# Kernel tuning notes

Measured on AMD Instinct MI355X. Metric: run time of the kernel, lower is better.

Reference implementation:

```python
import jax, jax.numpy as jnp
import numpy as np
import math

IMAGE_C = 1
IMAGE_W = 28
PIXELS_PER_ROW = IMAGE_W * IMAGE_C
NUM_HEADS = 8
TOP_K = 96
WINDOW_SIZE = 128
NEG_INF = -jnp.inf


def _causal_2d_mask(T):
    idx = jnp.arange(T)
    q_i = (idx // PIXELS_PER_ROW)[:, None]
    q_j = (idx % PIXELS_PER_ROW // IMAGE_C)[:, None]
    q_c = (idx % IMAGE_C)[:, None]
    k_i = (idx // PIXELS_PER_ROW)[None, :]
    k_j = (idx % PIXELS_PER_ROW // IMAGE_C)[None, :]
    k_c = (idx % IMAGE_C)[None, :]
    allowed = (k_i < q_i) | ((k_i == q_i) & (k_j < q_j)) | ((k_i == q_i) & (k_j == q_j) & (k_c <= q_c))
    return jnp.where(allowed, 0.0, NEG_INF)[None, None]  # [1,1,T,T]


def _window_mask(T, window_size):
    idx = jnp.arange(T)
    blocked = idx[None, :] < idx[:, None] - window_size + 1
    return jnp.where(blocked, NEG_INF, 0.0)[None, None]  # [1,1,T,T]


def setup_inputs() -> dict:
    key = jax.random.key(0)
    ks = jax.random.split(key, 10)
    B, T, E = 4, 2048, 512
    H = NUM_HEADS
    s = 0.02
    return {
        "x": jax.random.normal(ks[0], (B, T, E), jnp.float32),
        "Wq": jax.random.normal(ks[1], (E, E), jnp.float32) * s,
        "bq": jnp.zeros((E,), jnp.float32),
        "Wk": jax.random.normal(ks[2], (E, E), jnp.float32) * s,
        "bk": jnp.zeros((E,), jnp.float32),
        "Wv": jax.random.normal(ks[3], (E, E), jnp.float32) * s,
        "bv": jnp.zeros((E,), jnp.float32),
        "Wo": jax.random.normal(ks[4], (E, E), jnp.float32) * s,
        "bo": jnp.zeros((E,), jnp.float32),
        "log_sigma": jnp.full((H, 1, 1), math.log(2.5), jnp.float32),
    }


def reference(x, Wq, bq, Wk, bk, Wv, bv, Wo, bo, log_sigma):
    B, T, E = x.shape
    H = NUM_HEADS
    D = E // H

    def split_heads(y):  # [B,T,E] -> [B,H,T,D]
        return y.reshape(B, T, H, D).transpose(0, 2, 1, 3)

    q = split_heads(x @ Wq.T + bq)
    k = split_heads(x @ Wk.T + bk)
    v = split_heads(x @ Wv.T + bv)

    # Gaussian-kernel (squared-distance) scores: ||q-k||^2 / (-2 sigma^2)
    q_sq = jnp.sum(q * q, axis=-1, keepdims=True)            # [B,H,T,1]
    k_sq = jnp.sum(k * k, axis=-1, keepdims=True).transpose(0, 1, 3, 2)  # [B,H,1,T]
    product = jnp.einsum("bhqd,bhkd->bhqk", q, k)
    dist_sq = q_sq + k_sq - 2.0 * product
    sigma_sq = jnp.exp(2.0 * log_sigma)                       # [H,1,1]
    scores = dist_sq / (-2.0 * sigma_sq)

    scores = scores + _causal_2d_mask(T)
    if WINDOW_SIZE < T:
        scores = scores + _window_mask(T, WINDOW_SIZE)

    if TOP_K < T:
        K_val = min(TOP_K, T)
        # keep only the top-K scores per row (threshold at the K-th value);
        # equivalent to torch's gather/scatter for distinct finite scores
        top_vals = jax.lax.top_k(scores, K_val)[0]            # [B,H,T,K]
        kth = top_vals[..., -1:]
        scores = jnp.where(scores >= kth, scores, NEG_INF)

    probs = jax.nn.softmax(scores, axis=-1)                   # dropout = identity (eval)
    out = jnp.einsum("bhqk,bhkd->bhqd", probs, v)
    out = out.transpose(0, 2, 1, 3).reshape(B, T, E)
    return out @ Wo.T + bo
```

## Files before the change

### kernel.cpp

```cpp
#include <hip/hip_runtime.h>
#include <math.h>

#define T_SEQ   2048
#define EDIM    512
#define NHEADS  8
#define DHEAD   64
#define BATCH   4
#define WIN     128
#define TOPK    96

typedef _Float16 f16;
typedef f16 f16x2 __attribute__((ext_vector_type(2)));
typedef f16 f16x4 __attribute__((ext_vector_type(4)));
typedef f16 f16x8 __attribute__((ext_vector_type(8)));
typedef float f32x4 __attribute__((ext_vector_type(4)));

#define GLD_LDS(gp, lp) \
    __builtin_amdgcn_global_load_lds((const __attribute__((address_space(1))) void*)(gp), \
                                     (__attribute__((address_space(3))) void*)(lp), 16, 0, 0)

__global__ __launch_bounds__(256) void convert_all(
    const float* __restrict__ x,  const float* __restrict__ wq,
    const float* __restrict__ wk, const float* __restrict__ wv,
    const float* __restrict__ wo,
    f16* __restrict__ xh, f16* __restrict__ wqkvh, f16* __restrict__ woh)
{
    long i = ((long)blockIdx.x * 256 + threadIdx.x) * 4;
    const float* src; f16* dst; long off;
    if      (i < 4194304L) { src = x;  dst = xh;             off = i;            }
    else if (i < 4456448L) { src = wq; dst = wqkvh;          off = i - 4194304L; }
    else if (i < 4718592L) { src = wk; dst = wqkvh + 262144; off = i - 4456448L; }
    else if (i < 4980736L) { src = wv; dst = wqkvh + 524288; off = i - 4718592L; }
    else                   { src = wo; dst = woh;            off = i - 4980736L; }
    float4 v = *(const float4*)(src + off);
    f16x4 h; h.x = (f16)v.x; h.y = (f16)v.y; h.z = (f16)v.z; h.w = (f16)v.w;
    *(f16x4*)(dst + off) = h;
}

__global__ __launch_bounds__(256) void gemm_qkv(
    const f16* __restrict__ A, const f16* __restrict__ W,
    const float* __restrict__ b0, const float* __restrict__ b1,
    const float* __restrict__ b2,
    f16* __restrict__ cq, f16* __restrict__ ck, f16* __restrict__ cv)
{
    __shared__ f16 SH[16384];
    f16* Ash = SH;
    f16* Bsh = SH + 8192;

    const int tid  = threadIdx.x;
    const int w    = tid >> 6;
    const int lane = tid & 63;
    const int m0   = blockIdx.x * 128;
    const int n0   = blockIdx.y * 128;
    const int K    = 512;
    const int lr   = lane & 15;
    const int lk8  = (lane >> 4) * 8;

    f32x4 acc[4][4];
#pragma unroll
    for (int i = 0; i < 4; i++)
#pragma unroll
        for (int j = 0; j < 4; j++) acc[i][j] = (f32x4){0.f, 0.f, 0.f, 0.f};

    const int wmi = (w & 1) * 4;
    const int wni = (w >> 1) * 4;

    for (int k0 = 0; k0 < K; k0 += 64) {
#pragma unroll
        for (int cc = 0; cc < 4; cc++) {
            const int c  = w * 4 + cc;
            const int ms = c & 7, kp = c >> 3;
            const int kcol = k0 + kp * 32 + lk8;
            GLD_LDS(A + (size_t)(m0 + ms * 16 + lr) * K + kcol, Ash + c * 512);
            GLD_LDS(W + (size_t)(n0 + ms * 16 + lr) * K + kcol, Bsh + c * 512);
        }
        __syncthreads();

#pragma unroll
        for (int kp = 0; kp < 2; kp++) {
            f16x8 af[4], bf[4];
#pragma unroll
            for (int i = 0; i < 4; i++)
                af[i] = *(const f16x8*)(Ash + (kp * 8 + wmi + i) * 512 + lane * 8);
#pragma unroll
            for (int j = 0; j < 4; j++)
                bf[j] = *(const f16x8*)(Bsh + (kp * 8 + wni + j) * 512 + lane * 8);
#pragma unroll
            for (int i = 0; i < 4; i++)
#pragma unroll
                for (int j = 0; j < 4; j++)
                    acc[i][j] = __builtin_amdgcn_mfma_f32_16x16x32_f16(af[i], bf[j], acc[i][j], 0, 0, 0);
        }
        __syncthreads();
    }

    const int quad = lane >> 4;
    const int mat  = n0 >> 9;
    const float* bias = (mat == 0) ? b0 : ((mat == 1) ? b1 : b2);
    const int bb  = m0 >> 11;
    const int t0  = m0 & (T_SEQ - 1);
    const int hh0 = (n0 & 511) >> 6;

    if (mat < 2) {
#pragma unroll
        for (int i = 0; i < 4; i++) {
#pragma unroll
            for (int j = 0; j < 4; j++) {
                const int nl = (w >> 1) * 64 + j * 16 + lr;
                const float bvv = bias[(n0 & 511) + nl];
#pragma unroll
                for (int r = 0; r < 4; r++) {
                    const int ml = (w & 1) * 64 + i * 16 + quad * 4 + r;
                    SH[ml * 128 + (nl ^ (((ml >> 2) & 7) << 4))] = (f16)(acc[i][j][r] + bvv);
                }
            }
        }
        __syncthreads();
        f16* dst = (mat == 0) ? cq : ck;
#pragma unroll
        for (int s = 0; s < 8; s++) {
            const int c   = tid + 256 * s;
            const int row = c >> 4;
            const int nt  = (c & 15) * 8;
            const f16x8 vv = *(const f16x8*)&SH[row * 128 + (nt ^ (((row >> 2) & 7) << 4))];
            const int hh = hh0 + (nt >> 6);
            const int dd = nt & 63;
            *(f16x8*)(dst + ((size_t)((bb * NHEADS + hh) * T_SEQ) + t0 + row) * 64 + dd) = vv;
        }
    } else {
#pragma unroll
        for (int i = 0; i < 4; i++) {
#pragma unroll
            for (int j = 0; j < 4; j++) {
                const int nl = (w >> 1) * 64 + j * 16 + lr;
                const float bvv = bias[(n0 & 511) + nl];
                const int mlb = (w & 1) * 64 + i * 16 + quad * 4;
                f16x4 pk;
#pragma unroll
                for (int r = 0; r < 4; r++) pk[r] = (f16)(acc[i][j][r] + bvv);
                *(f16x4*)&SH[nl * 128 + ((mlb + 8 * (nl & 15)) & 127)] = pk;
            }
        }
        __syncthreads();
#pragma unroll
        for (int s = 0; s < 8; s++) {
            const int c    = tid + 256 * s;
            const int nrow = c >> 4;
            const int cht  = c & 15;
            const int chl  = (cht + (nrow & 15)) & 15;
            const f16x8 vv = *(const f16x8*)&SH[nrow * 128 + chl * 8];
            const int hh = hh0 + (nrow >> 6);
            const int dd = nrow & 63;
            *(f16x8*)(cv + ((size_t)((bb * NHEADS + hh) * 64 + dd)) * T_SEQ + t0 + cht * 8) = vv;
        }
    }
}

__global__ __launch_bounds__(256) void gemm_o(
    const f16* __restrict__ A, const f16* __restrict__ W,
    const float* __restrict__ bias, float* __restrict__ C)
{
    __shared__ __align__(16) char SMO[34816];
    f16*   Ash = (f16*)SMO;
    f16*   Bsh = (f16*)(SMO + 16384);
    float* SC  = (float*)SMO;

    const int tid  = threadIdx.x;
    const int w    = tid >> 6;
    const int lane = tid & 63;
    const int m0   = blockIdx.x * 128;
    const int n0   = blockIdx.y * 64;
    const int lr   = lane & 15;
    const int lk8  = (lane >> 4) * 8;

    f32x4 acc[4][2];
#pragma unroll
    for (int i = 0; i < 4; i++)
#pragma unroll
        for (int j = 0; j < 2; j++) acc[i][j] = (f32x4){0.f, 0.f, 0.f, 0.f};

    for (int k0 = 0; k0 < 512; k0 += 64) {
#pragma unroll
        for (int cc = 0; cc < 4; cc++) {
            const int c  = w * 4 + cc;
            const int ms = c & 7, kp = c >> 3;
            GLD_LDS(A + (size_t)(m0 + ms * 16 + lr) * 512 + k0 + kp * 32 + lk8, Ash + c * 512);
        }
#pragma unroll
        for (int cc = 0; cc < 2; cc++) {
            const int c  = w * 2 + cc;
            const int ns = c & 3, kp = c >> 2;
            GLD_LDS(W + (size_t)(n0 + ns * 16 + lr) * 512 + k0 + kp * 32 + lk8, Bsh + c * 512);
        }
        __syncthreads();

#pragma unroll
        for (int kp = 0; kp < 2; kp++) {
            f16x8 af[4], bf[2];
#pragma unroll
            for (int i = 0; i < 4; i++)
                af[i] = *(const f16x8*)(Ash + (kp * 8 + (w & 1) * 4 + i) * 512 + lane * 8);
#pragma unroll
            for (int j = 0; j < 2; j++)
                bf[j] = *(const f16x8*)(Bsh + (kp * 4 + (w >> 1) * 2 + j) * 512 + lane * 8);
#pragma unroll
            for (int i = 0; i < 4; i++)
#pragma unroll
                for (int j = 0; j < 2; j++)
                    acc[i][j] = __builtin_amdgcn_mfma_f32_16x16x32_f16(af[i], bf[j], acc[i][j], 0, 0, 0);
        }
        __syncthreads();
    }

    const int quad = lane >> 4;
#pragma unroll
    for (int i = 0; i < 4; i++) {
#pragma unroll
        for (int j = 0; j < 2; j++) {
            const int n  = (w >> 1) * 32 + j * 16 + lr;
            const float bv = bias[n0 + n];
#pragma unroll
            for (int r = 0; r < 4; r++) {
                const int m = (w & 1) * 64 + i * 16 + quad * 4 + r;
                SC[m * 68 + n] = acc[i][j][r] + bv;
            }
        }
    }
    __syncthreads();
#pragma unroll
    for (int s = 0; s < 8; s++) {
        const int c   = tid + 256 * s;
        const int row = c >> 4;
        const int nt  = (c & 15) * 4;
        const f32x4 vv = *(const f32x4*)&SC[row * 68 + nt];
        *(f32x4*)&C[(size_t)(m0 + row) * 512 + n0 + nt] = vv;
    }
}

__global__ __launch_bounds__(512, 4) void attn_v5(
    const f16* __restrict__ qh, const f16* __restrict__ kh,
    const f16* __restrict__ vtg, const float* __restrict__ logsig,
    f16* __restrict__ abh)
{
    __shared__ __align__(16) char smem[79616];
    f16*   Qs   = (f16*)smem;
    f16*   Ks   = (f16*)(smem + 11264);
    f16*   P    = (f16*)smem;
    float* Sc   = (float*)(smem + 45056);
    f16*   Vt   = (f16*)(smem + 45056);
    float* ksqs = (float*)(smem + 78848);

    const int tid = threadIdx.x, w = tid >> 6, lane = tid & 63;
    const int lr = lane & 15, quad = lane >> 4;
    const int q0 = blockIdx.x * 64, bh = blockIdx.y;
    const int h = bh & 7, b = bh >> 3;
    const size_t tb = (size_t)bh * T_SEQ;
    const int ks0 = q0 - 128;

    {
        const int row = tid >> 3, ch = tid & 7;
        f16x8 v = *(const f16x8*)(qh + (tb + q0 + row) * 64 + ch * 8);
        *(f16x8*)(Qs + row * 88 + ch * 8) = v;
    }
#pragma unroll
    for (int s = 0; s < 3; s++) {
        const int i = tid + 512 * s;
        const int row = i >> 3, ch = i & 7;
        const int kg = ks0 + row;
        f16x8 v = {};
        if (kg >= 0) v = *(const f16x8*)(kh + (tb + kg) * 64 + ch * 8);
        *(f16x8*)(Ks + row * 88 + ch * 8) = v;
        float ps = 0.f;
#pragma unroll
        for (int j = 0; j < 8; j++) { const float fv = (float)v[j]; ps += fv * fv; }
        ps += __shfl_xor(ps, 1);
        ps += __shfl_xor(ps, 2);
        ps += __shfl_xor(ps, 4);
        if (ch == 0) ksqs[row] = ps;
    }
    __syncthreads();

    const int mt  = w & 3;
    const int kh2 = w >> 2;
    f32x4 accQ[6];
#pragma unroll
    for (int jt = 0; jt < 6; jt++) accQ[jt] = (f32x4){0.f, 0.f, 0.f, 0.f};

    __builtin_amdgcn_s_setprio(1);
#pragma unroll
    for (int kp = 0; kp < 2; kp++) {
        const f16x8 af = *(const f16x8*)(Qs + (mt * 16 + lr) * 88 + kp * 32 + quad * 8);
#pragma unroll
        for (int jt = 0; jt < 6; jt++) {
            const f16x8 bf = *(const f16x8*)(Ks + (kh2 * 96 + jt * 16 + lr) * 88 + kp * 32 + quad * 8);
            accQ[jt] = __builtin_amdgcn_mfma_f32_16x16x32_f16(af, bf, accQ[jt], 0, 0, 0);
        }
    }
    __builtin_amdgcn_s_setprio(0);
    const float inv_s2 = __expf(-2.0f * logsig[h]);
#pragma unroll
    for (int jt = 0; jt < 6; jt++) {
        const int c  = kh2 * 96 + jt * 16 + lr;
        const float kq = ksqs[c];
        const int kg = ks0 + c;
#pragma unroll
        for (int r = 0; r < 4; r++) {
            const int dq = mt * 16 + quad * 4 + r;
            const unsigned wc = (unsigned)(c - dq - 1);
            if (wc < 128u) {
                Sc[dq * 132 + wc] = (kg >= 0) ? (accQ[jt][r] - 0.5f * kq) * inv_s2
                                              : -INFINITY;
            }
        }
    }

    f16x8 vpre[3];
#pragma unroll
    for (int s = 0; s < 3; s++) {
        const int i = tid + 512 * s;
        const int d = i / 24, ch = i % 24;
        const int t0v = ks0 + ch * 8;
        f16x8 vv = {};
        if (t0v >= 0) vv = *(const f16x8*)(vtg + ((size_t)bh * 64 + d) * T_SEQ + t0v);
        vpre[s] = vv;
    }
    __syncthreads();

    const int wq8 = w * 8;
#pragma unroll 1
    for (int g = 0; g < 2; g++) {
        const int dq0 = wq8 + g * 4;
        float s0[4], s1[4], m[4];
        unsigned u0[4], u1[4], t[4];
#pragma unroll
        for (int qq = 0; qq < 4; qq++) {
            const int dq = dq0 + qq;
            s0[qq] = Sc[dq * 132 + lane];
            s1[qq] = Sc[dq * 132 + 64 + lane];
            const unsigned b0 = __float_as_uint(s0[qq]);
            const unsigned b1 = __float_as_uint(s1[qq]);
            u0[qq] = b0 ^ (unsigned)(((int)b0 >> 31) | 0x80000000);
            u1[qq] = b1 ^ (unsigned)(((int)b1 >> 31) | 0x80000000);
            m[qq] = __uint_as_float(__builtin_amdgcn_readlane(__float_as_uint(s1[qq]), 63));
            t[qq] = 0u;
        }
#pragma unroll
        for (int bit = 31; bit >= 0; bit--) {
#pragma unroll
            for (int qq = 0; qq < 4; qq++) {
                const unsigned c = t[qq] | (1u << bit);
                const int n = __popcll(__ballot(u0[qq] >= c)) +
                              __popcll(__ballot(u1[qq] >= c));
                if (n >= TOPK) t[qq] = c;
            }
        }
#pragma unroll
        for (int qq = 0; qq < 4; qq++) {
            const int dq = dq0 + qq;
            const float p0 = (u0[qq] >= t[qq]) ? __expf(s0[qq] - m[qq]) : 0.f;
            const float p1 = (u1[qq] >= t[qq]) ? __expf(s1[qq] - m[qq]) : 0.f;
            P[dq * 216 + dq + 1 + lane]  = (f16)p0;
            P[dq * 216 + dq + 65 + lane] = (f16)p1;
            P[dq * 216 + ((lane <= dq) ? lane : lane + 128)] = (f16)0.f;
        }
    }
    __syncthreads();

#pragma unroll
    for (int s = 0; s < 3; s++) {
        const int i = tid + 512 * s;
        const int d = i / 24, ch = i % 24;
        *(f16x8*)(Vt + d * 216 + ch * 8) = vpre[s];
    }
    __syncthreads();

    const int nh = w >> 2;
    f32x4 accO[2];
#pragma unroll
    for (int nt = 0; nt < 2; nt++) accO[nt] = (f32x4){0.f, 0.f, 0.f, 0.f};
    f32x4 accS = (f32x4){0.f, 0.f, 0.f, 0.f};
    f16x8 onesf;
#pragma unroll
    for (int j = 0; j < 8; j++) onesf[j] = (f16)1.0f;

    __builtin_amdgcn_s_setprio(1);
#pragma unroll
    for (int ks = 0; ks < 6; ks++) {
        const f16x8 pf = *(const f16x8*)(P + (mt * 16 + lr) * 216 + ks * 32 + quad * 8);
#pragma unroll
        for (int nt = 0; nt < 2; nt++) {
            const f16x8 vf = *(const f16x8*)(Vt + (nh * 32 + nt * 16 + lr) * 216 + ks * 32 + quad * 8);
            accO[nt] = __builtin_amdgcn_mfma_f32_16x16x32_f16(pf, vf, accO[nt], 0, 0, 0);
        }
        accS = __builtin_amdgcn_mfma_f32_16x16x32_f16(pf, onesf, accS, 0, 0, 0);
    }
    __builtin_amdgcn_s_setprio(0);
    float inv[4];
#pragma unroll
    for (int r = 0; r < 4; r++) inv[r] = 1.0f / accS[r];

#pragma unroll
    for (int nt = 0; nt < 2; nt++) {
        const int d = nh * 32 + nt * 16 + lr;
#pragma unroll
        for (int r = 0; r < 4; r++) {
            const int q = q0 + mt * 16 + quad * 4 + r;
            abh[((size_t)(b * T_SEQ + q)) * 512 + h * 64 + d] = (f16)(accO[nt][r] * inv[r]);
        }
    }
}

extern "C" void kernel_launch(void* const* d_in, const int* in_sizes, int n_in,
                              void* d_out, int out_size, void* d_ws, size_t ws_size,
                              hipStream_t stream)
{
    const float* x      = (const float*)d_in[0];
    const float* Wq     = (const float*)d_in[1];
    const float* bq     = (const float*)d_in[2];
    const float* Wk     = (const float*)d_in[3];
    const float* bk     = (const float*)d_in[4];
    const float* Wv     = (const float*)d_in[5];
    const float* bv     = (const float*)d_in[6];
    const float* Wo     = (const float*)d_in[7];
    const float* bo     = (const float*)d_in[8];
    const float* logsig = (const float*)d_in[9];

    f16* xh    = (f16*)d_ws;
    f16* wqkvh = xh + 4194304;
    f16* woh   = wqkvh + 786432;
    f16* qh    = woh + 262144;
    f16* kh    = qh + 4194304;
    f16* vtg   = kh + 4194304;
    f16* abh   = xh;

    convert_all<<<5120, 256, 0, stream>>>(x, Wq, Wk, Wv, Wo, xh, wqkvh, woh);

    gemm_qkv<<<dim3(64, 12), 256, 0, stream>>>(xh, wqkvh, bq, bk, bv, qh, kh, vtg);

    attn_v5<<<dim3(T_SEQ / 64, BATCH * NHEADS), 512, 0, stream>>>(
        qh, kh, vtg, logsig, abh);

    gemm_o<<<dim3(64, 8), 256, 0, stream>>>(abh, woh, bo, (float*)d_out);
}
```

Measured before the change: 173.0 us.

## Shrink attention LDS footprint by aliasing score buffer to raise occupancy

The attention kernel now reuses the Q/K region for the score matrix and packs P/Vt with a tighter row stride, cutting shared memory from about 78KB to about 51KB per block. Launch bounds are raised to request 6 blocks per CU. To make the aliasing legal, the scores are first loaded into registers as sortable keys, followed by a barrier, and only then does the top-k bit search run and write P. The cost is an extra barrier, more live registers holding keys across the barrier, and a different LDS stride that may change bank conflicts.

```diff
diff --git a/kernel.cpp b/kernel.cpp
--- a/kernel.cpp
+++ b/kernel.cpp
@@ -237,18 +237,24 @@
     }
 }
 
-__global__ __launch_bounds__(512, 4) void attn_v5(
+__device__ __forceinline__ float keyinv(unsigned u)
+{
+    unsigned b = u ^ ((unsigned)((int)(~u) >> 31) | 0x80000000u);
+    return __uint_as_float(b);
+}
+
+__global__ __launch_bounds__(512, 6) void attn_v6(
     const f16* __restrict__ qh, const f16* __restrict__ kh,
     const f16* __restrict__ vtg, const float* __restrict__ logsig,
     f16* __restrict__ abh)
 {
-    __shared__ __align__(16) char smem[79616];
+    __shared__ __align__(16) char smem[51968];
     f16*   Qs   = (f16*)smem;
     f16*   Ks   = (f16*)(smem + 11264);
+    float* Sc   = (float*)smem;
     f16*   P    = (f16*)smem;
-    float* Sc   = (float*)(smem + 45056);
-    f16*   Vt   = (f16*)(smem + 45056);
-    float* ksqs = (float*)(smem + 78848);
+    f16*   Vt   = (f16*)(smem + 25600);
+    float* ksqs = (float*)(smem + 51200);
 
     const int tid = threadIdx.x, w = tid >> 6, lane = tid & 63;
     const int lr = lane & 15, quad = lane >> 4;
@@ -297,6 +303,8 @@
         }
     }
     __builtin_amdgcn_s_setprio(0);
+    __syncthreads();
+
     const float inv_s2 = __expf(-2.0f * logsig[h]);
 #pragma unroll
     for (int jt = 0; jt < 6; jt++) {
@@ -327,41 +335,20 @@
     __syncthreads();
 
     const int wq8 = w * 8;
-#pragma unroll 1
+    unsigned u0[2][4], u1[2][4];
+    float mx[2][4];
+#pragma unroll
     for (int g = 0; g < 2; g++) {
-        const int dq0 = wq8 + g * 4;
-        float s0[4], s1[4], m[4];
-        unsigned u0[4], u1[4], t[4];
 #pragma unroll
         for (int qq = 0; qq < 4; qq++) {
-            const int dq = dq0 + qq;
-            s0[qq] = Sc[dq * 132 + lane];
-            s1[qq] = Sc[dq * 132 + 64 + lane];
-            const unsigned b0 = __float_as_uint(s0[qq]);
-            const unsigned b1 = __float_as_uint(s1[qq]);
-            u0[qq] = b0 ^ (unsigned)(((int)b0 >> 31) | 0x80000000);
-            u1[qq] = b1 ^ (unsigned)(((int)b1 >> 31) | 0x80000000);
-            m[qq] = __uint_as_float(__builtin_amdgcn_readlane(__float_as_uint(s1[qq]), 63));
-            t[qq] = 0u;
-        }
-#pragma unroll
-        for (int bit = 31; bit >= 0; bit--) {
-#pragma unroll
-            for (int qq = 0; qq < 4; qq++) {
-                const unsigned c = t[qq] | (1u << bit);
-                const int n = __popcll(__ballot(u0[qq] >= c)) +
-                              __popcll(__ballot(u1[qq] >= c));
-                if (n >= TOPK) t[qq] = c;
-            }
-        }
-#pragma unroll
-        for (int qq = 0; qq < 4; qq++) {
-            const int dq = dq0 + qq;
-            const float p0 = (u0[qq] >= t[qq]) ? __expf(s0[qq] - m[qq]) : 0.f;
-            const float p1 = (u1[qq] >= t[qq]) ? __expf(s1[qq] - m[qq]) : 0.f;
-            P[dq * 216 + dq + 1 + lane]  = (f16)p0;
-            P[dq * 216 + dq + 65 + lane] = (f16)p1;
-            P[dq * 216 + ((lane <= dq) ? lane : lane + 128)] = (f16)0.f;
+            const int dq = wq8 + g * 4 + qq;
+            const float s0 = Sc[dq * 132 + lane];
+            const float s1 = Sc[dq * 132 + 64 + lane];
+            const unsigned b0 = __float_as_uint(s0);
+            const unsigned b1 = __float_as_uint(s1);
+            u0[g][qq] = b0 ^ (unsigned)(((int)b0 >> 31) | 0x80000000);
+            u1[g][qq] = b1 ^ (unsigned)(((int)b1 >> 31) | 0x80000000);
+            mx[g][qq] = __uint_as_float(__builtin_amdgcn_readlane(__float_as_uint(s1), 63));
         }
     }
     __syncthreads();
@@ -370,7 +357,35 @@
     for (int s = 0; s < 3; s++) {
         const int i = tid + 512 * s;
         const int d = i / 24, ch = i % 24;
-        *(f16x8*)(Vt + d * 216 + ch * 8) = vpre[s];
+        *(f16x8*)(Vt + d * 200 + ch * 8) = vpre[s];
+    }
+
+#pragma unroll 1
+    for (int g = 0; g < 2; g++) {
+        unsigned t[4];
+#pragma unroll
+        for (int qq = 0; qq < 4; qq++) t[qq] = 0u;
+#pragma unroll
+        for (int bit = 31; bit >= 0; bit--) {
+#pragma unroll
+            for (int qq = 0; qq < 4; qq++) {
+                const unsigned c = t[qq] | (1u << bit);
+                const int n = __popcll(__ballot(u0[g][qq] >= c)) +
+                              __popcll(__ballot(u1[g][qq] >= c));
+                if (n >= TOPK) t[qq] = c;
+            }
+        }
+#pragma unroll
+        for (int qq = 0; qq < 4; qq++) {
+            const int dq = wq8 + g * 4 + qq;
+            const float s0 = keyinv(u0[g][qq]);
+            const float s1 = keyinv(u1[g][qq]);
+            const float p0 = (u0[g][qq] >= t[qq]) ? __expf(s0 - mx[g][qq]) : 0.f;
+            const float p1 = (u1[g][qq] >= t[qq]) ? __expf(s1 - mx[g][qq]) : 0.f;
+            P[dq * 200 + dq + 1 + lane]  = (f16)p0;
+            P[dq * 200 + dq + 65 + lane] = (f16)p1;
+            P[dq * 200 + ((lane <= dq) ? lane : lane + 128)] = (f16)0.f;
+        }
     }
     __syncthreads();
 
@@ -386,10 +401,10 @@
     __builtin_amdgcn_s_setprio(1);
 #pragma unroll
     for (int ks = 0; ks < 6; ks++) {
-        const f16x8 pf = *(const f16x8*)(P + (mt * 16 + lr) * 216 + ks * 32 + quad * 8);
+        const f16x8 pf = *(const f16x8*)(P + (mt * 16 + lr) * 200 + ks * 32 + quad * 8);
 #pragma unroll
         for (int nt = 0; nt < 2; nt++) {
-            const f16x8 vf = *(const f16x8*)(Vt + (nh * 32 + nt * 16 + lr) * 216 + ks * 32 + quad * 8);
+            const f16x8 vf = *(const f16x8*)(Vt + (nh * 32 + nt * 16 + lr) * 200 + ks * 32 + quad * 8);
             accO[nt] = __builtin_amdgcn_mfma_f32_16x16x32_f16(pf, vf, accO[nt], 0, 0, 0);
         }
         accS = __builtin_amdgcn_mfma_f32_16x16x32_f16(pf, onesf, accS, 0, 0, 0);
@@ -437,7 +452,7 @@
 
     gemm_qkv<<<dim3(64, 12), 256, 0, stream>>>(xh, wqkvh, bq, bk, bv, qh, kh, vtg);
 
-    attn_v5<<<dim3(T_SEQ / 64, BATCH * NHEADS), 512, 0, stream>>>(
+    attn_v6<<<dim3(T_SEQ / 64, BATCH * NHEADS), 512, 0, stream>>>(
         qh, kh, vtg, logsig, abh);
 
     gemm_o<<<dim3(64, 8), 256, 0, stream>>>(abh, woh, bo, (float*)d_out);
```

Result: slower. 192.2 us (+11.1%).
